# Optimization experiments

Measured on AMD Instinct MI355X. Metric: run time of the kernel, lower is better.

The kernel has to match this reference:

```python
import jax, jax.numpy as jnp
import numpy as np

N_NODES = 100000   # n_nodes
N_EDGES = 1600000  # n_nodes * avg_degree(16)
D_IN = 128
D_OUT = 128


def setup_inputs() -> dict:
    key = jax.random.key(0)
    k1, k2, k3, k4, k5 = jax.random.split(key, 5)
    h = jax.random.normal(k1, (N_NODES, D_IN), dtype=jnp.float32)
    edge_src = jax.random.randint(k2, (N_EDGES,), 0, N_NODES, dtype=jnp.int32)
    edge_dst = jax.random.randint(k3, (N_EDGES,), 0, N_NODES, dtype=jnp.int32)
    # Linear params, init per reset_parameters: U(-stdv, stdv), stdv = 1/sqrt(in_feats)
    stdv = 1.0 / np.sqrt(D_IN)
    W = jax.random.uniform(k4, (D_OUT, D_IN), dtype=jnp.float32, minval=-stdv, maxval=stdv)
    b = jax.random.uniform(k5, (D_OUT,), dtype=jnp.float32, minval=-stdv, maxval=stdv)
    return {"h": h, "edge_src": edge_src, "edge_dst": edge_dst, "W": W, "b": b}


def reference(h, edge_src, edge_dst, W, b):
    # update_all(copy_src('h'), sum) == neighbor-sum aggregation (SpMM with 0/1 adjacency)
    ah = jax.ops.segment_sum(h[edge_src], edge_dst, num_segments=N_NODES)  # [N, D_IN]
    # dense linear + activation fused on the aggregated features
    return jax.nn.relu(ah @ W.T + b)  # [N, D_OUT]
```

## Files before the change

### kernel.cpp

```cpp
#include <hip/hip_runtime.h>

#define D 128
#define BKT_SHIFT 9
#define BKT_SIZE 512
#define P1_EPB 4096
#define CNT_EPB 2048
#define SW_LDU 68

typedef __attribute__((ext_vector_type(8))) short bf16x8;
typedef __attribute__((ext_vector_type(4))) float f32x4;

__device__ inline unsigned int pack2bf(float a, float b) {
    unsigned int ua = __float_as_uint(a);
    unsigned int ub = __float_as_uint(b);
    ua = (ua + 0x7fffu + ((ua >> 16) & 1u)) >> 16;
    ub = (ub + 0x7fffu + ((ub >> 16) & 1u)) >> 16;
    return ua | (ub << 16);
}
__device__ inline unsigned short pack1bf(float a) {
    unsigned int ua = __float_as_uint(a);
    return (unsigned short)((ua + 0x7fffu + ((ua >> 16) & 1u)) >> 16);
}


__global__ __launch_bounds__(256) void bucket_count_kernel(
    const int* __restrict__ edst, int* __restrict__ bucketCnt, int n_edges, int nbk)
{
    __shared__ int hcnt[256];
    const int tid = threadIdx.x;
    hcnt[tid] = 0;
    __syncthreads();
    const int base = blockIdx.x * CNT_EPB;
    const int lim = min(CNT_EPB, n_edges - base);
    int k = tid;
    for (; k + 768 < lim; k += 1024) {
        int d0 = edst[base + k];
        int d1 = edst[base + k + 256];
        int d2 = edst[base + k + 512];
        int d3 = edst[base + k + 768];
        atomicAdd(&hcnt[d0 >> BKT_SHIFT], 1);
        atomicAdd(&hcnt[d1 >> BKT_SHIFT], 1);
        atomicAdd(&hcnt[d2 >> BKT_SHIFT], 1);
        atomicAdd(&hcnt[d3 >> BKT_SHIFT], 1);
    }
    for (; k < lim; k += 256)
        atomicAdd(&hcnt[edst[base + k] >> BKT_SHIFT], 1);
    __syncthreads();
    if (tid < nbk && hcnt[tid] > 0) atomicAdd(&bucketCnt[tid], hcnt[tid]);
}

__global__ __launch_bounds__(256) void bucket_scan_kernel(
    const int* __restrict__ bucketCnt, int* __restrict__ bucketBase,
    int* __restrict__ bucketCur, int nbk)
{
    __shared__ int s[256];
    const int t = threadIdx.x;
    int v = (t < nbk) ? bucketCnt[t] : 0;
    s[t] = v;
    __syncthreads();
    #pragma unroll
    for (int off = 1; off < 256; off <<= 1) {
        int x = (t >= off) ? s[t - off] : 0;
        __syncthreads();
        s[t] += x;
        __syncthreads();
    }
    if (t < nbk) {
        int base = s[t] - v;
        bucketBase[t] = base;
        bucketCur[t] = base;
    }
}

__global__ __launch_bounds__(256) void p1_partition_kernel(
    const int* __restrict__ esrc, const int* __restrict__ edst,
    int* __restrict__ bucketCur, unsigned int* __restrict__ pairs, int n_edges)
{
    __shared__ int hist[256];
    __shared__ int lbase[256];
    __shared__ int gbase[256];
    __shared__ int cur[256];
    __shared__ unsigned int buf[P1_EPB];
    __shared__ unsigned char bkt8[P1_EPB];
    const int tid = threadIdx.x;
    const int base = blockIdx.x * P1_EPB;
    hist[tid] = 0;
    __syncthreads();
    unsigned int pk[16]; int bk[16];
    #pragma unroll
    for (int k = 0; k < 16; k++) {
        int e = base + k * 256 + tid;
        if (e < n_edges) {
            int sv = esrc[e], dv = edst[e];
            bk[k] = dv >> BKT_SHIFT;
            pk[k] = ((unsigned)sv << BKT_SHIFT) | (unsigned)(dv & (BKT_SIZE - 1));
            atomicAdd(&hist[bk[k]], 1);
        } else bk[k] = -1;
    }
    __syncthreads();
    const int v = hist[tid];
    if (v > 0) gbase[tid] = atomicAdd(&bucketCur[tid], v);
    lbase[tid] = v;
    __syncthreads();
    #pragma unroll
    for (int off = 1; off < 256; off <<= 1) {
        int x = (tid >= off) ? lbase[tid - off] : 0;
        __syncthreads();
        lbase[tid] += x;
        __syncthreads();
    }
    const int excl = lbase[tid] - v;
    __syncthreads();
    lbase[tid] = excl;
    cur[tid] = excl;
    __syncthreads();
    #pragma unroll
    for (int k = 0; k < 16; k++) {
        if (bk[k] >= 0) {
            int loc = atomicAdd(&cur[bk[k]], 1);
            buf[loc] = pk[k];
            bkt8[loc] = (unsigned char)bk[k];
        }
    }
    __syncthreads();
    const int total = min(P1_EPB, n_edges - base);
    for (int i = tid; i < total; i += 256) {
        int b = bkt8[i];
        pairs[gbase[b] + (i - lbase[b])] = buf[i];
    }
}

__global__ __launch_bounds__(256) void p2_sort_gemm_kernel(
    const unsigned int* __restrict__ pairs, const int* __restrict__ bucketBase,
    int* __restrict__ sorted_src, int* __restrict__ gstart, int* __restrict__ gend,
    const float* __restrict__ h, const float* __restrict__ W,
    unsigned short* __restrict__ z,
    int n_nodes, int n_edges, int nbk)
{
    __shared__ union SU {
        struct { int hist[BKT_SIZE]; int cur[BKT_SIZE]; int sb[256]; } s;
        unsigned int sW[128 * SW_LDU];
    } u;
    const int tid = threadIdx.x;

    if ((int)blockIdx.x < nbk) {
        const int bkt = blockIdx.x;
        const int nbase = bkt << BKT_SHIFT;
        const int pstart = bucketBase[bkt];
        const int pend = (bkt == nbk - 1) ? n_edges : bucketBase[bkt + 1];
        u.s.hist[tid] = 0; u.s.hist[tid + 256] = 0;
        __syncthreads();
        {
            int j = pstart + tid;
            for (; j + 768 < pend; j += 1024) {
                unsigned int q0 = pairs[j];
                unsigned int q1 = pairs[j + 256];
                unsigned int q2 = pairs[j + 512];
                unsigned int q3 = pairs[j + 768];
                atomicAdd(&u.s.hist[q0 & (BKT_SIZE - 1)], 1);
                atomicAdd(&u.s.hist[q1 & (BKT_SIZE - 1)], 1);
                atomicAdd(&u.s.hist[q2 & (BKT_SIZE - 1)], 1);
                atomicAdd(&u.s.hist[q3 & (BKT_SIZE - 1)], 1);
            }
            for (; j < pend; j += 256)
                atomicAdd(&u.s.hist[pairs[j] & (BKT_SIZE - 1)], 1);
        }
        __syncthreads();
        int a  = u.s.hist[2 * tid];
        int b2 = u.s.hist[2 * tid + 1];
        int psum = a + b2;
        u.s.sb[tid] = psum;
        __syncthreads();
        #pragma unroll
        for (int off = 1; off < 256; off <<= 1) {
            int x = (tid >= off) ? u.s.sb[tid - off] : 0;
            __syncthreads();
            u.s.sb[tid] += x;
            __syncthreads();
        }
        int pexcl = u.s.sb[tid] - psum;
        u.s.cur[2 * tid] = pexcl;
        u.s.cur[2 * tid + 1] = pexcl + a;
        __syncthreads();
        for (int i = tid; i < BKT_SIZE; i += 256) {
            int nd = nbase + i;
            if (nd < n_nodes) {
                int st = pstart + u.s.cur[i];
                gstart[nd] = st;
                gend[nd] = st + u.s.hist[i];
            }
        }
        __syncthreads();
        {
            int j = pstart + tid;
            for (; j + 768 < pend; j += 1024) {
                unsigned int q0 = pairs[j];
                unsigned int q1 = pairs[j + 256];
                unsigned int q2 = pairs[j + 512];
                unsigned int q3 = pairs[j + 768];
                int p0 = pstart + atomicAdd(&u.s.cur[q0 & (BKT_SIZE - 1)], 1);
                int p1 = pstart + atomicAdd(&u.s.cur[q1 & (BKT_SIZE - 1)], 1);
                int p2 = pstart + atomicAdd(&u.s.cur[q2 & (BKT_SIZE - 1)], 1);
                int p3 = pstart + atomicAdd(&u.s.cur[q3 & (BKT_SIZE - 1)], 1);
                sorted_src[p0] = (int)(q0 >> BKT_SHIFT);
                sorted_src[p1] = (int)(q1 >> BKT_SHIFT);
                sorted_src[p2] = (int)(q2 >> BKT_SHIFT);
                sorted_src[p3] = (int)(q3 >> BKT_SHIFT);
            }
            for (; j < pend; j += 256) {
                unsigned int p = pairs[j];
                int local = p & (BKT_SIZE - 1);
                int pos = pstart + atomicAdd(&u.s.cur[local], 1);
                sorted_src[pos] = (int)(p >> BKT_SHIFT);
            }
        }
    } else {
        const int gbid = blockIdx.x - nbk;
        for (int i = tid; i < 4096; i += 256) {
            float4 w = ((const float4*)W)[i];
            int row = i >> 5, c4 = i & 31;
            unsigned int* dst = &u.sW[row * SW_LDU + c4 * 2];
            dst[0] = pack2bf(w.x, w.y);
            dst[1] = pack2bf(w.z, w.w);
        }
        __syncthreads();

        const int wave = tid >> 6;
        const int lane = tid & 63;
        const int m = lane & 15;
        const int q = lane >> 4;
        const int r0 = gbid * 64 + wave * 16;
        const int arow = r0 + m;
        const bool rvalid = arow < n_nodes;

        bf16x8 afrag[4];
        #pragma unroll
        for (int ks = 0; ks < 4; ks++) {
            float4 x = make_float4(0.f, 0.f, 0.f, 0.f), y = x;
            if (rvalid) {
                const float4* p = (const float4*)(h + (size_t)arow * D + ks * 32 + q * 8);
                x = p[0]; y = p[1];
            }
            union { unsigned int uu[4]; bf16x8 v; } cvt;
            cvt.uu[0] = pack2bf(x.x, x.y);
            cvt.uu[1] = pack2bf(x.z, x.w);
            cvt.uu[2] = pack2bf(y.x, y.y);
            cvt.uu[3] = pack2bf(y.z, y.w);
            afrag[ks] = cvt.v;
        }

        f32x4 acc[8];
        #pragma unroll
        for (int ct = 0; ct < 8; ct++) acc[ct] = (f32x4){0.f, 0.f, 0.f, 0.f};

        #pragma unroll
        for (int ct = 0; ct < 8; ct++) {
            #pragma unroll
            for (int ks = 0; ks < 4; ks++) {
                const unsigned int* p = &u.sW[(ct * 16 + m) * SW_LDU + ks * 16 + q * 4];
                union { uint4 uu; bf16x8 v; } bu;
                bu.uu = *(const uint4*)p;
                acc[ct] = __builtin_amdgcn_mfma_f32_16x16x32_bf16(afrag[ks], bu.v, acc[ct], 0, 0, 0);
            }
        }

        #pragma unroll
        for (int ct = 0; ct < 8; ct++) {
            int col = ct * 16 + m;
            #pragma unroll
            for (int i = 0; i < 4; i++) {
                int r = r0 + q * 4 + i;
                if (r < n_nodes) z[(size_t)r * D + col] = pack1bf(acc[ct][i]);
            }
        }
    }
}

__global__ __launch_bounds__(256) void p2_sort_kernel(
    const unsigned int* __restrict__ pairs, const int* __restrict__ bucketBase,
    int* __restrict__ sorted_src, int* __restrict__ gstart, int* __restrict__ gend,
    int n_nodes, int n_edges, int nbk)
{
    __shared__ int hist[BKT_SIZE];
    __shared__ int cur[BKT_SIZE];
    __shared__ int sb[256];
    const int tid = threadIdx.x;
    const int bkt = blockIdx.x;
    const int nbase = bkt << BKT_SHIFT;
    const int pstart = bucketBase[bkt];
    const int pend = (bkt == nbk - 1) ? n_edges : bucketBase[bkt + 1];
    hist[tid] = 0; hist[tid + 256] = 0;
    __syncthreads();
    for (int j = pstart + tid; j < pend; j += 256)
        atomicAdd(&hist[pairs[j] & (BKT_SIZE - 1)], 1);
    __syncthreads();
    int a  = hist[2 * tid];
    int b2 = hist[2 * tid + 1];
    int psum = a + b2;
    sb[tid] = psum;
    __syncthreads();
    #pragma unroll
    for (int off = 1; off < 256; off <<= 1) {
        int x = (tid >= off) ? sb[tid - off] : 0;
        __syncthreads();
        sb[tid] += x;
        __syncthreads();
    }
    int pexcl = sb[tid] - psum;
    cur[2 * tid] = pexcl;
    cur[2 * tid + 1] = pexcl + a;
    __syncthreads();
    for (int i = tid; i < BKT_SIZE; i += 256) {
        int nd = nbase + i;
        if (nd < n_nodes) {
            int st = pstart + cur[i];
            gstart[nd] = st;
            gend[nd] = st + hist[i];
        }
    }
    __syncthreads();
    for (int j = pstart + tid; j < pend; j += 256) {
        unsigned int p = pairs[j];
        int local = p & (BKT_SIZE - 1);
        int pos = pstart + atomicAdd(&cur[local], 1);
        sorted_src[pos] = (int)(p >> BKT_SHIFT);
    }
}

__global__ __launch_bounds__(256) void gemm_z_kernel(
    const float* __restrict__ h, const float* __restrict__ W,
    unsigned short* __restrict__ z, int n_nodes)
{
    __shared__ unsigned int sW[128 * SW_LDU];
    const int tid = threadIdx.x;
    for (int i = tid; i < 4096; i += 256) {
        float4 w = ((const float4*)W)[i];
        int row = i >> 5, c4 = i & 31;
        unsigned int* dst = &sW[row * SW_LDU + c4 * 2];
        dst[0] = pack2bf(w.x, w.y);
        dst[1] = pack2bf(w.z, w.w);
    }
    __syncthreads();

    const int wave = tid >> 6;
    const int lane = tid & 63;
    const int m = lane & 15;
    const int q = lane >> 4;
    const int r0 = blockIdx.x * 64 + wave * 16;
    const int arow = r0 + m;
    const bool rvalid = arow < n_nodes;

    bf16x8 afrag[4];
    #pragma unroll
    for (int ks = 0; ks < 4; ks++) {
        float4 x = make_float4(0.f, 0.f, 0.f, 0.f), y = x;
        if (rvalid) {
            const float4* p = (const float4*)(h + (size_t)arow * D + ks * 32 + q * 8);
            x = p[0]; y = p[1];
        }
        union { unsigned int u[4]; bf16x8 v; } cvt;
        cvt.u[0] = pack2bf(x.x, x.y);
        cvt.u[1] = pack2bf(x.z, x.w);
        cvt.u[2] = pack2bf(y.x, y.y);
        cvt.u[3] = pack2bf(y.z, y.w);
        afrag[ks] = cvt.v;
    }

    f32x4 acc[8];
    #pragma unroll
    for (int ct = 0; ct < 8; ct++) acc[ct] = (f32x4){0.f, 0.f, 0.f, 0.f};

    #pragma unroll
    for (int ct = 0; ct < 8; ct++) {
        #pragma unroll
        for (int ks = 0; ks < 4; ks++) {
            const unsigned int* p = &sW[(ct * 16 + m) * SW_LDU + ks * 16 + q * 4];
            union { uint4 u; bf16x8 v; } bu;
            bu.u = *(const uint4*)p;
            acc[ct] = __builtin_amdgcn_mfma_f32_16x16x32_bf16(afrag[ks], bu.v, acc[ct], 0, 0, 0);
        }
    }

    #pragma unroll
    for (int ct = 0; ct < 8; ct++) {
        int col = ct * 16 + m;
        #pragma unroll
        for (int i = 0; i < 4; i++) {
            int r = r0 + q * 4 + i;
            if (r < n_nodes) z[(size_t)r * D + col] = pack1bf(acc[ct][i]);
        }
    }
}

__global__ __launch_bounds__(256) void gather_row_kernel(
    const unsigned short* __restrict__ z, const int* __restrict__ gstart,
    const int* __restrict__ gend, const int* __restrict__ sorted_src,
    const float* __restrict__ b, float* __restrict__ out, int n_nodes,
    int node_base)
{
    const int tid = threadIdx.x;
    const int node = node_base + blockIdx.x * 16 + (tid >> 4);
    const int lane = tid & 15;
    if (node >= n_nodes) return;
    int e = gstart[node];
    const int end = gend[node];
    const uint4* __restrict__ z4 = (const uint4*)z;
    float acc[8];
    #pragma unroll
    for (int i = 0; i < 8; i++) acc[i] = 0.f;
#define ADDV(v) do { \
    acc[0] += __uint_as_float((v).x << 16); acc[1] += __uint_as_float((v).x & 0xffff0000u); \
    acc[2] += __uint_as_float((v).y << 16); acc[3] += __uint_as_float((v).y & 0xffff0000u); \
    acc[4] += __uint_as_float((v).z << 16); acc[5] += __uint_as_float((v).z & 0xffff0000u); \
    acc[6] += __uint_as_float((v).w << 16); acc[7] += __uint_as_float((v).w & 0xffff0000u); } while (0)
    for (; e + 4 <= end; e += 4) {
        int s0 = sorted_src[e + 0];
        int s1 = sorted_src[e + 1];
        int s2 = sorted_src[e + 2];
        int s3 = sorted_src[e + 3];
        uint4 v0 = z4[(size_t)s0 * 16 + lane];
        uint4 v1 = z4[(size_t)s1 * 16 + lane];
        uint4 v2 = z4[(size_t)s2 * 16 + lane];
        uint4 v3 = z4[(size_t)s3 * 16 + lane];
        ADDV(v0); ADDV(v1); ADDV(v2); ADDV(v3);
    }
    for (; e < end; e++) {
        uint4 v = z4[(size_t)sorted_src[e] * 16 + lane];
        ADDV(v);
    }
#undef ADDV
    float4 b0 = ((const float4*)b)[lane * 2];
    float4 b1 = ((const float4*)b)[lane * 2 + 1];
    float4* o = (float4*)(out + (size_t)node * D + lane * 8);
    o[0] = make_float4(fmaxf(acc[0] + b0.x, 0.f), fmaxf(acc[1] + b0.y, 0.f),
                       fmaxf(acc[2] + b0.z, 0.f), fmaxf(acc[3] + b0.w, 0.f));
    o[1] = make_float4(fmaxf(acc[4] + b1.x, 0.f), fmaxf(acc[5] + b1.y, 0.f),
                       fmaxf(acc[6] + b1.z, 0.f), fmaxf(acc[7] + b1.w, 0.f));
}


__global__ __launch_bounds__(256) void hist_kernel(
    const int* __restrict__ edst, int* __restrict__ cnt, int n_edges)
{
    int gid = blockIdx.x * 256 + threadIdx.x;
    if (gid < n_edges) atomicAdd(&cnt[edst[gid]], 1);
}

__global__ __launch_bounds__(256) void scanA_kernel(
    const int* __restrict__ cnt, int* __restrict__ localoff,
    int* __restrict__ blocksums, int n)
{
    __shared__ int s[256];
    const int t = threadIdx.x;
    const int base = blockIdx.x * 1024 + t * 4;
    int v[4]; int sum = 0;
    #pragma unroll
    for (int i = 0; i < 4; i++) {
        int idx = base + i;
        v[i] = (idx < n) ? cnt[idx] : 0;
        sum += v[i];
    }
    s[t] = sum;
    __syncthreads();
    #pragma unroll
    for (int off = 1; off < 256; off <<= 1) {
        int x = (t >= off) ? s[t - off] : 0;
        __syncthreads();
        s[t] += x;
        __syncthreads();
    }
    int excl = s[t] - sum;
    int run = 0;
    #pragma unroll
    for (int i = 0; i < 4; i++) {
        int idx = base + i;
        if (idx < n) localoff[idx] = excl + run;
        run += v[i];
    }
    if (t == 255) blocksums[blockIdx.x] = s[255];
}

__global__ __launch_bounds__(256) void scanB_kernel(
    const int* __restrict__ blocksums, int* __restrict__ blockoffs, int nb)
{
    __shared__ int s[256];
    const int t = threadIdx.x;
    int v = (t < nb) ? blocksums[t] : 0;
    s[t] = v;
    __syncthreads();
    #pragma unroll
    for (int off = 1; off < 256; off <<= 1) {
        int x = (t >= off) ? s[t - off] : 0;
        __syncthreads();
        s[t] += x;
        __syncthreads();
    }
    if (t < nb) blockoffs[t] = s[t] - v;
}

__global__ __launch_bounds__(256) void scanC_kernel(
    const int* __restrict__ localoff, const int* __restrict__ blockoffs,
    int* __restrict__ outoffs, int* __restrict__ cursor, int n)
{
    int gid = blockIdx.x * 256 + threadIdx.x;
    if (gid >= n) return;
    int v = localoff[gid] + blockoffs[blockIdx.x >> 2];
    outoffs[gid] = v;
    if (cursor) cursor[gid] = v;
}

__global__ __launch_bounds__(256) void place_kernel(
    const int* __restrict__ esrc, const int* __restrict__ edst,
    int* __restrict__ cursor, int* __restrict__ sorted_src, int n_edges)
{
    int gid = blockIdx.x * 256 + threadIdx.x;
    if (gid >= n_edges) return;
    int d = edst[gid];
    int pos = atomicAdd(&cursor[d], 1);
    sorted_src[pos] = esrc[gid];
}

__global__ __launch_bounds__(256) void gather_kernel(
    const float* __restrict__ h, const int* __restrict__ offs,
    const int* __restrict__ endp, const int* __restrict__ sorted_src,
    float* __restrict__ out, int n_nodes)
{
    const int tid = threadIdx.x;
    const int node = blockIdx.x * 8 + (tid >> 5);
    const int lane = tid & 31;
    if (node >= n_nodes) return;
    const int start = offs[node];
    const int end = endp[node];
    const float4* __restrict__ h4 = (const float4*)h;
    float4 acc = make_float4(0.f, 0.f, 0.f, 0.f);
    for (int e = start; e < end; e++) {
        float4 a = h4[(size_t)sorted_src[e] * 32 + lane];
        acc.x += a.x; acc.y += a.y; acc.z += a.z; acc.w += a.w;
    }
    ((float4*)out)[(size_t)node * 32 + lane] = acc;
}

__global__ __launch_bounds__(256) void scatter_kernel(
    const float* __restrict__ h, const int* __restrict__ esrc,
    const int* __restrict__ edst, float* __restrict__ out, int n_edges)
{
    int gid = blockIdx.x * 256 + threadIdx.x;
    int e = gid >> 5;
    int l = gid & 31;
    if (e >= n_edges) return;
    int s = esrc[e];
    int d = edst[e];
    float4 v = ((const float4*)(h + (size_t)s * D))[l];
    float* o = out + (size_t)d * D + (size_t)l * 4;
    atomicAdd(o + 0, v.x);
    atomicAdd(o + 1, v.y);
    atomicAdd(o + 2, v.z);
    atomicAdd(o + 3, v.w);
}

__global__ __launch_bounds__(256) void mfma_gemm_relu_kernel(
    float* __restrict__ io, const float* __restrict__ W,
    const float* __restrict__ b, int n_nodes)
{
    __shared__ unsigned int sW[128 * SW_LDU];
    const int tid = threadIdx.x;
    for (int i = tid; i < 4096; i += 256) {
        float4 w = ((const float4*)W)[i];
        int row = i >> 5, c4 = i & 31;
        unsigned int* dst = &sW[row * SW_LDU + c4 * 2];
        dst[0] = pack2bf(w.x, w.y);
        dst[1] = pack2bf(w.z, w.w);
    }
    __syncthreads();
    const int wave = tid >> 6;
    const int lane = tid & 63;
    const int m = lane & 15;
    const int q = lane >> 4;
    const int r0 = blockIdx.x * 64 + wave * 16;
    const int arow = r0 + m;
    const bool rvalid = arow < n_nodes;
    bf16x8 afrag[4];
    #pragma unroll
    for (int ks = 0; ks < 4; ks++) {
        float4 x = make_float4(0.f, 0.f, 0.f, 0.f), y = x;
        if (rvalid) {
            const float4* p = (const float4*)(io + (size_t)arow * D + ks * 32 + q * 8);
            x = p[0]; y = p[1];
        }
        union { unsigned int u[4]; bf16x8 v; } cvt;
        cvt.u[0] = pack2bf(x.x, x.y);
        cvt.u[1] = pack2bf(x.z, x.w);
        cvt.u[2] = pack2bf(y.x, y.y);
        cvt.u[3] = pack2bf(y.z, y.w);
        afrag[ks] = cvt.v;
    }
    f32x4 acc[8];
    #pragma unroll
    for (int ct = 0; ct < 8; ct++) acc[ct] = (f32x4){0.f, 0.f, 0.f, 0.f};
    #pragma unroll
    for (int ct = 0; ct < 8; ct++) {
        #pragma unroll
        for (int ks = 0; ks < 4; ks++) {
            const unsigned int* p = &sW[(ct * 16 + m) * SW_LDU + ks * 16 + q * 4];
            union { uint4 u; bf16x8 v; } bu;
            bu.u = *(const uint4*)p;
            acc[ct] = __builtin_amdgcn_mfma_f32_16x16x32_bf16(afrag[ks], bu.v, acc[ct], 0, 0, 0);
        }
    }
    #pragma unroll
    for (int ct = 0; ct < 8; ct++) {
        int col = ct * 16 + m;
        float bias = b[col];
        #pragma unroll
        for (int i = 0; i < 4; i++) {
            int r = r0 + q * 4 + i;
            if (r < n_nodes) {
                float v = acc[ct][i] + bias;
                io[(size_t)r * D + col] = v > 0.f ? v : 0.f;
            }
        }
    }
}

extern "C" void kernel_launch(void* const* d_in, const int* in_sizes, int n_in,
                              void* d_out, int out_size, void* d_ws, size_t ws_size,
                              hipStream_t stream) {
    const float* h    = (const float*)d_in[0];
    const int*   esrc = (const int*)d_in[1];
    const int*   edst = (const int*)d_in[2];
    const float* W    = (const float*)d_in[3];
    const float* b    = (const float*)d_in[4];
    float* out = (float*)d_out;
    const int n_nodes = in_sizes[0] / D;
    const int n_edges = in_sizes[1];
    const int NB  = (n_nodes + 1023) / 1024;
    const int NBK = (n_nodes + BKT_SIZE - 1) / BKT_SIZE;

    size_t fixed = ((size_t)2 * n_nodes + 3 * NBK + (size_t)n_edges) * 4;
    size_t pairs_off = (fixed + 15) & ~(size_t)15;
    size_t z_off = (pairs_off + (size_t)n_edges * 4 + 15) & ~(size_t)15;
    size_t need_fused = z_off + (size_t)n_nodes * D * 2;

    size_t zone_bytes = (size_t)n_edges * 4;
    size_t zb2 = (size_t)n_nodes * D * 2;
    if (zb2 > zone_bytes) zone_bytes = zb2;
    size_t need_main = pairs_off + zone_bytes;

    if (ws_size >= need_fused && NBK <= 256 && n_nodes <= (1 << 22)) {
        int* gstart     = (int*)d_ws;
        int* gend       = gstart + n_nodes;
        int* bucketCnt  = gend + n_nodes;
        int* bucketBase = bucketCnt + NBK;
        int* bucketCur  = bucketBase + NBK;
        int* sorted_src = bucketCur + NBK;
        unsigned int* pairs = (unsigned int*)((char*)d_ws + pairs_off);
        unsigned short* z   = (unsigned short*)((char*)d_ws + z_off);

        hipMemsetAsync(bucketCnt, 0, (size_t)NBK * sizeof(int), stream);
        bucket_count_kernel<<<(n_edges + CNT_EPB - 1) / CNT_EPB, 256, 0, stream>>>(
            edst, bucketCnt, n_edges, NBK);
        bucket_scan_kernel<<<1, 256, 0, stream>>>(bucketCnt, bucketBase, bucketCur, NBK);
        p1_partition_kernel<<<(n_edges + P1_EPB - 1) / P1_EPB, 256, 0, stream>>>(
            esrc, edst, bucketCur, pairs, n_edges);
        const int gemmBlocks = (n_nodes + 63) / 64;
        p2_sort_gemm_kernel<<<NBK + gemmBlocks, 256, 0, stream>>>(
            pairs, bucketBase, sorted_src, gstart, gend, h, W, z,
            n_nodes, n_edges, NBK);
        const int half = (n_nodes + 1) / 2;
        const int haligned = ((half + 15) / 16) * 16;
        gather_row_kernel<<<(haligned + 15) / 16, 256, 0, stream>>>(
            z, gstart, gend, sorted_src, b, out, min(haligned, n_nodes), 0);
        if (n_nodes > haligned)
            gather_row_kernel<<<(n_nodes - haligned + 15) / 16, 256, 0, stream>>>(
                z, gstart, gend, sorted_src, b, out, n_nodes, haligned);
        return;
    }

    if (ws_size >= need_main && NBK <= 256 && n_nodes <= (1 << 23)) {
        int* gstart     = (int*)d_ws;
        int* gend       = gstart + n_nodes;
        int* bucketCnt  = gend + n_nodes;
        int* bucketBase = bucketCnt + NBK;
        int* bucketCur  = bucketBase + NBK;
        int* sorted_src = bucketCur + NBK;
        void* zone = (char*)d_ws + pairs_off;
        unsigned int* pairs = (unsigned int*)zone;
        unsigned short* z = (unsigned short*)zone;

        hipMemsetAsync(bucketCnt, 0, (size_t)NBK * sizeof(int), stream);
        bucket_count_kernel<<<(n_edges + CNT_EPB - 1) / CNT_EPB, 256, 0, stream>>>(
            edst, bucketCnt, n_edges, NBK);
        bucket_scan_kernel<<<1, 256, 0, stream>>>(bucketCnt, bucketBase, bucketCur, NBK);
        p1_partition_kernel<<<(n_edges + P1_EPB - 1) / P1_EPB, 256, 0, stream>>>(
            esrc, edst, bucketCur, pairs, n_edges);
        p2_sort_kernel<<<NBK, 256, 0, stream>>>(
            pairs, bucketBase, sorted_src, gstart, gend, n_nodes, n_edges, NBK);
        gemm_z_kernel<<<(n_nodes + 63) / 64, 256, 0, stream>>>(h, W, z, n_nodes);
        gather_row_kernel<<<(n_nodes + 15) / 16, 256, 0, stream>>>(
            z, gstart, gend, sorted_src, b, out, n_nodes, 0);
        return;
    }

    size_t csr_ints = (size_t)3 * n_nodes + 2 * NB + (size_t)n_edges;
    size_t needB = csr_ints * sizeof(int);
    if (ws_size >= needB && NB <= 256) {
        int* cnt        = (int*)d_ws;
        int* offs       = cnt + n_nodes;
        int* cursor     = offs + n_nodes;
        int* blocksums  = cursor + n_nodes;
        int* blockoffs  = blocksums + NB;
        int* sorted_src = blockoffs + NB;

        hipMemsetAsync(cnt, 0, (size_t)n_nodes * sizeof(int), stream);
        hist_kernel<<<(n_edges + 255) / 256, 256, 0, stream>>>(edst, cnt, n_edges);
        scanA_kernel<<<NB, 256, 0, stream>>>(cnt, offs, blocksums, n_nodes);
        scanB_kernel<<<1, 256, 0, stream>>>(blocksums, blockoffs, NB);
        scanC_kernel<<<(n_nodes + 255) / 256, 256, 0, stream>>>(
            offs, blockoffs, cnt, cursor, n_nodes);
        place_kernel<<<(n_edges + 255) / 256, 256, 0, stream>>>(
            esrc, edst, cursor, sorted_src, n_edges);
        gather_kernel<<<(n_nodes + 7) / 8, 256, 0, stream>>>(
            h, cnt, cursor, sorted_src, out, n_nodes);
    } else {
        hipMemsetAsync(out, 0, (size_t)n_nodes * D * sizeof(float), stream);
        long long total = (long long)n_edges * 32;
        scatter_kernel<<<(int)((total + 255) / 256), 256, 0, stream>>>(h, esrc, edst, out, n_edges);
    }
    mfma_gemm_relu_kernel<<<(n_nodes + 63) / 64, 256, 0, stream>>>(out, W, b, n_nodes);
}
```

Baseline: 255.4 us.

## Replace count atomics with per-block partials, stage GEMM output via LDS, merge gather launches

Bucket counting now writes per-block partial histograms to a fixed 256-block partials array, and the scan kernel sums them. This removes the memset and the global atomics. The GEMM epilogues stage bf16 results in LDS and then write 16-byte coalesced rows to z instead of scattered 2-byte stores. The two half-size gather launches are merged into one. The trade-off is a serial 256-iteration sum in the single-block scan and fewer, larger count blocks.

```diff
diff --git a/kernel.cpp b/kernel.cpp
--- a/kernel.cpp
+++ b/kernel.cpp
@@ -4,7 +4,8 @@
 #define BKT_SHIFT 9
 #define BKT_SIZE 512
 #define P1_EPB 4096
-#define CNT_EPB 2048
+#define CNT_BLOCKS 256
+#define PARTIALS_INTS (256 * 256)
 #define SW_LDU 68
 
 typedef __attribute__((ext_vector_type(8))) short bf16x8;
@@ -24,14 +25,14 @@
 
 
 __global__ __launch_bounds__(256) void bucket_count_kernel(
-    const int* __restrict__ edst, int* __restrict__ bucketCnt, int n_edges, int nbk)
+    const int* __restrict__ edst, int* __restrict__ partials, int n_edges, int epb)
 {
     __shared__ int hcnt[256];
     const int tid = threadIdx.x;
     hcnt[tid] = 0;
     __syncthreads();
-    const int base = blockIdx.x * CNT_EPB;
-    const int lim = min(CNT_EPB, n_edges - base);
+    const int base = blockIdx.x * epb;
+    const int lim = min(epb, n_edges - base);
     int k = tid;
     for (; k + 768 < lim; k += 1024) {
         int d0 = edst[base + k];
@@ -46,16 +47,19 @@
     for (; k < lim; k += 256)
         atomicAdd(&hcnt[edst[base + k] >> BKT_SHIFT], 1);
     __syncthreads();
-    if (tid < nbk && hcnt[tid] > 0) atomicAdd(&bucketCnt[tid], hcnt[tid]);
+    partials[(blockIdx.x << 8) + tid] = hcnt[tid];
 }
 
 __global__ __launch_bounds__(256) void bucket_scan_kernel(
-    const int* __restrict__ bucketCnt, int* __restrict__ bucketBase,
+    const int* __restrict__ partials, int* __restrict__ bucketBase,
     int* __restrict__ bucketCur, int nbk)
 {
     __shared__ int s[256];
     const int t = threadIdx.x;
-    int v = (t < nbk) ? bucketCnt[t] : 0;
+    int sum = 0;
+    #pragma unroll 8
+    for (int b = 0; b < CNT_BLOCKS; b++) sum += partials[(b << 8) + t];
+    int v = (t < nbk) ? sum : 0;
     s[t] = v;
     __syncthreads();
     #pragma unroll
@@ -264,13 +268,30 @@
             }
         }
 
+        __syncthreads();
+        unsigned short* lds_us = (unsigned short*)u.sW;
         #pragma unroll
         for (int ct = 0; ct < 8; ct++) {
-            int col = ct * 16 + m;
             #pragma unroll
             for (int i = 0; i < 4; i++) {
-                int r = r0 + q * 4 + i;
-                if (r < n_nodes) z[(size_t)r * D + col] = pack1bf(acc[ct][i]);
+                lds_us[(wave * 16 + q * 4 + i) * 130 + ct * 16 + m] = pack1bf(acc[ct][i]);
+            }
+        }
+        __syncthreads();
+        const unsigned int* lds32 = (const unsigned int*)u.sW;
+        const int r0blk = gbid * 64;
+        #pragma unroll
+        for (int pass = 0; pass < 4; pass++) {
+            int idx = pass * 256 + tid;
+            int row = idx >> 4;
+            int c16 = idx & 15;
+            int r = r0blk + row;
+            if (r < n_nodes) {
+                int bo = row * 65 + c16 * 4;
+                uint4 val;
+                val.x = lds32[bo]; val.y = lds32[bo + 1];
+                val.z = lds32[bo + 2]; val.w = lds32[bo + 3];
+                ((uint4*)z)[(size_t)r * 16 + c16] = val;
             }
         }
     }
@@ -381,13 +402,30 @@
         }
     }
 
+    __syncthreads();
+    unsigned short* lds_us = (unsigned short*)sW;
     #pragma unroll
     for (int ct = 0; ct < 8; ct++) {
-        int col = ct * 16 + m;
         #pragma unroll
         for (int i = 0; i < 4; i++) {
-            int r = r0 + q * 4 + i;
-            if (r < n_nodes) z[(size_t)r * D + col] = pack1bf(acc[ct][i]);
+            lds_us[(wave * 16 + q * 4 + i) * 130 + ct * 16 + m] = pack1bf(acc[ct][i]);
+        }
+    }
+    __syncthreads();
+    const unsigned int* lds32 = (const unsigned int*)sW;
+    const int r0blk = blockIdx.x * 64;
+    #pragma unroll
+    for (int pass = 0; pass < 4; pass++) {
+        int idx = pass * 256 + tid;
+        int row = idx >> 4;
+        int c16 = idx & 15;
+        int r = r0blk + row;
+        if (r < n_nodes) {
+            int bo = row * 65 + c16 * 4;
+            uint4 val;
+            val.x = lds32[bo]; val.y = lds32[bo + 1];
+            val.z = lds32[bo + 2]; val.w = lds32[bo + 3];
+            ((uint4*)z)[(size_t)r * 16 + c16] = val;
         }
     }
 }
@@ -636,7 +674,7 @@
     const int NB  = (n_nodes + 1023) / 1024;
     const int NBK = (n_nodes + BKT_SIZE - 1) / BKT_SIZE;
 
-    size_t fixed = ((size_t)2 * n_nodes + 3 * NBK + (size_t)n_edges) * 4;
+    size_t fixed = ((size_t)2 * n_nodes + PARTIALS_INTS + 2 * NBK + (size_t)n_edges) * 4;
     size_t pairs_off = (fixed + 15) & ~(size_t)15;
     size_t z_off = (pairs_off + (size_t)n_edges * 4 + 15) & ~(size_t)15;
     size_t need_fused = z_off + (size_t)n_nodes * D * 2;
@@ -646,51 +684,46 @@
     if (zb2 > zone_bytes) zone_bytes = zb2;
     size_t need_main = pairs_off + zone_bytes;
 
+    const int cnt_epb = (n_edges + CNT_BLOCKS - 1) / CNT_BLOCKS;
+
     if (ws_size >= need_fused && NBK <= 256 && n_nodes <= (1 << 22)) {
         int* gstart     = (int*)d_ws;
         int* gend       = gstart + n_nodes;
-        int* bucketCnt  = gend + n_nodes;
-        int* bucketBase = bucketCnt + NBK;
+        int* partials   = gend + n_nodes;
+        int* bucketBase = partials + PARTIALS_INTS;
         int* bucketCur  = bucketBase + NBK;
         int* sorted_src = bucketCur + NBK;
         unsigned int* pairs = (unsigned int*)((char*)d_ws + pairs_off);
         unsigned short* z   = (unsigned short*)((char*)d_ws + z_off);
 
-        hipMemsetAsync(bucketCnt, 0, (size_t)NBK * sizeof(int), stream);
-        bucket_count_kernel<<<(n_edges + CNT_EPB - 1) / CNT_EPB, 256, 0, stream>>>(
-            edst, bucketCnt, n_edges, NBK);
-        bucket_scan_kernel<<<1, 256, 0, stream>>>(bucketCnt, bucketBase, bucketCur, NBK);
+        bucket_count_kernel<<<CNT_BLOCKS, 256, 0, stream>>>(
+            edst, partials, n_edges, cnt_epb);
+        bucket_scan_kernel<<<1, 256, 0, stream>>>(partials, bucketBase, bucketCur, NBK);
         p1_partition_kernel<<<(n_edges + P1_EPB - 1) / P1_EPB, 256, 0, stream>>>(
             esrc, edst, bucketCur, pairs, n_edges);
         const int gemmBlocks = (n_nodes + 63) / 64;
         p2_sort_gemm_kernel<<<NBK + gemmBlocks, 256, 0, stream>>>(
             pairs, bucketBase, sorted_src, gstart, gend, h, W, z,
             n_nodes, n_edges, NBK);
-        const int half = (n_nodes + 1) / 2;
-        const int haligned = ((half + 15) / 16) * 16;
-        gather_row_kernel<<<(haligned + 15) / 16, 256, 0, stream>>>(
-            z, gstart, gend, sorted_src, b, out, min(haligned, n_nodes), 0);
-        if (n_nodes > haligned)
-            gather_row_kernel<<<(n_nodes - haligned + 15) / 16, 256, 0, stream>>>(
-                z, gstart, gend, sorted_src, b, out, n_nodes, haligned);
+        gather_row_kernel<<<(n_nodes + 15) / 16, 256, 0, stream>>>(
+            z, gstart, gend, sorted_src, b, out, n_nodes, 0);
         return;
     }
 
     if (ws_size >= need_main && NBK <= 256 && n_nodes <= (1 << 23)) {
         int* gstart     = (int*)d_ws;
         int* gend       = gstart + n_nodes;
-        int* bucketCnt  = gend + n_nodes;
-        int* bucketBase = bucketCnt + NBK;
+        int* partials   = gend + n_nodes;
+        int* bucketBase = partials + PARTIALS_INTS;
         int* bucketCur  = bucketBase + NBK;
         int* sorted_src = bucketCur + NBK;
         void* zone = (char*)d_ws + pairs_off;
         unsigned int* pairs = (unsigned int*)zone;
         unsigned short* z = (unsigned short*)zone;
 
-        hipMemsetAsync(bucketCnt, 0, (size_t)NBK * sizeof(int), stream);
-        bucket_count_kernel<<<(n_edges + CNT_EPB - 1) / CNT_EPB, 256, 0, stream>>>(
-            edst, bucketCnt, n_edges, NBK);
-        bucket_scan_kernel<<<1, 256, 0, stream>>>(bucketCnt, bucketBase, bucketCur, NBK);
+        bucket_count_kernel<<<CNT_BLOCKS, 256, 0, stream>>>(
+            edst, partials, n_edges, cnt_epb);
+        bucket_scan_kernel<<<1, 256, 0, stream>>>(partials, bucketBase, bucketCur, NBK);
         p1_partition_kernel<<<(n_edges + P1_EPB - 1) / P1_EPB, 256, 0, stream>>>(
             esrc, edst, bucketCur, pairs, n_edges);
         p2_sort_kernel<<<NBK, 256, 0, stream>>>(
```

New measurement: 236.2 us. 1.08x faster.
